# Kernel tuning notes

Hardware: AMD Instinct MI355X
Metric: run time of the kernel (lower is better)

Reference implementation:

```python
import jax, jax.numpy as jnp
import numpy as np

B, N, M, C, T, HF, WF = 4, 512, 32, 512, 8, 14, 14
K = 80          # num_classes
P = 7           # ROI pool output size
HID = 1024
IMG = 224


def setup_inputs() -> dict:
    key = jax.random.key(0)
    k0, k1, k2, k3, k4, k5 = jax.random.split(key, 6)
    feature = jax.random.normal(k0, (B, C, T, HF, WF), dtype=jnp.float32)
    # GT boxes: realistic xyxy boxes inside a 224x224 image
    ka, kb = jax.random.split(k1)
    cxy = jax.random.uniform(ka, (B, M, 2), minval=40.0, maxval=180.0)
    wh = jax.random.uniform(kb, (B, M, 2), minval=40.0, maxval=100.0)
    gt_bboxes = jnp.concatenate([cxy - wh / 2, cxy + wh / 2], axis=-1).astype(jnp.float32)
    # Proposals: jittered copies of GT boxes so many pass the IoU>=0.85 fg test
    idx = jnp.arange(N) % M
    base = gt_bboxes[:, idx]                                   # [B,N,4]
    noise = jax.random.normal(k2, (B, N, 4), dtype=jnp.float32) * 1.5
    proposal_bboxes = jnp.clip(base + noise, 0.0, float(IMG))
    gt_classes = (jax.random.uniform(k3, (B, M, K)) < 0.1).astype(jnp.float32)
    W1 = jax.random.normal(k4, (C * P * P, HID), dtype=jnp.float32) * 0.01
    b1 = jnp.zeros((HID,), jnp.float32)
    W2 = jax.random.normal(k5, (HID, K), dtype=jnp.float32) * 0.01
    b2 = jnp.zeros((K,), jnp.float32)
    return {"feature": feature, "proposal_bboxes": proposal_bboxes,
            "gt_bboxes": gt_bboxes, "gt_classes": gt_classes,
            "W1": W1, "b1": b1, "W2": W2, "b2": b2,
            "image_h": IMG, "image_w": IMG}


def _iou(a, b):
    # a [B,N,4], b [B,M,4] xyxy -> [B,N,M]
    lt = jnp.maximum(a[:, :, None, :2], b[:, None, :, :2])
    rb = jnp.minimum(a[:, :, None, 2:], b[:, None, :, 2:])
    wh = jnp.clip(rb - lt, 0.0)
    inter = wh[..., 0] * wh[..., 1]
    area_a = (a[..., 2] - a[..., 0]) * (a[..., 3] - a[..., 1])
    area_b = (b[..., 2] - b[..., 0]) * (b[..., 3] - b[..., 1])
    return inter / (area_a[:, :, None] + area_b[:, None, :] - inter + 1e-8)


def _roi_pool(feat_bhwc, boxes, bidx, sy, sx):
    # feat_bhwc [B,H,W,C]; boxes [R,4] image coords; bilinear 7x7 ROI pooling
    H, W = feat_bhwc.shape[1], feat_bhwc.shape[2]
    x1, y1, x2, y2 = boxes[:, 0] * sx, boxes[:, 1] * sy, boxes[:, 2] * sx, boxes[:, 3] * sy
    g = (jnp.arange(P, dtype=jnp.float32) + 0.5) / P
    ys = y1[:, None] + g[None, :] * (y2 - y1)[:, None]        # [R,P]
    xs = x1[:, None] + g[None, :] * (x2 - x1)[:, None]        # [R,P]
    y = jnp.broadcast_to(ys[:, :, None], (boxes.shape[0], P, P)) - 0.5
    x = jnp.broadcast_to(xs[:, None, :], (boxes.shape[0], P, P)) - 0.5
    y0f = jnp.floor(y); x0f = jnp.floor(x)
    wy = jnp.clip(y - y0f, 0.0, 1.0)[..., None]
    wx = jnp.clip(x - x0f, 0.0, 1.0)[..., None]
    y0 = jnp.clip(y0f, 0, H - 1).astype(jnp.int32)
    y1i = jnp.clip(y0f + 1, 0, H - 1).astype(jnp.int32)
    x0 = jnp.clip(x0f, 0, W - 1).astype(jnp.int32)
    x1i = jnp.clip(x0f + 1, 0, W - 1).astype(jnp.int32)
    bi = bidx[:, None, None]
    gather = lambda yy, xx: feat_bhwc[bi, yy, xx]             # [R,P,P,C]
    out = (gather(y0, x0) * (1 - wy) * (1 - wx) + gather(y0, x1i) * (1 - wy) * wx +
           gather(y1i, x0) * wy * (1 - wx) + gather(y1i, x1i) * wy * wx)
    return out


def reference(feature, proposal_bboxes, gt_bboxes, gt_classes, W1, b1, W2, b2, image_h, image_w):
    # temporal average pool (AvgPool3d over T) -> [B,C,HF,WF]
    feat = feature.mean(axis=2)
    feat_bhwc = jnp.transpose(feat, (0, 2, 3, 1))             # [B,HF,WF,C]
    # IoU-based fg assignment
    ious = _iou(proposal_bboxes, gt_bboxes)                   # [B,N,M]
    max_iou = ious.max(axis=2)                                # [B,N]
    assign = ious.argmax(axis=2)                              # [B,N]
    any_fg = jnp.any(max_iou >= 0.85)
    thresh = jnp.where(any_fg, 0.85, 0.5)                     # fallback branch
    fg = (max_iou >= thresh).astype(feature.dtype)            # [B,N]
    # ROI pool all proposals (bg masked out in the loss)
    boxes = proposal_bboxes.reshape(B * N, 4)
    bidx = jnp.repeat(jnp.arange(B, dtype=jnp.int32), N)
    sy = feat.shape[2] / float(image_h)
    sx = feat.shape[3] / float(image_w)
    pool = _roi_pool(feat_bhwc, boxes, bidx, sy, sx)          # [R,P,P,C]
    pool = jnp.transpose(pool, (0, 3, 1, 2)).reshape(B * N, C * P * P)
    hidden = jax.nn.relu(pool @ W1 + b1)                      # [R,HID]
    logits = hidden @ W2 + b2                                 # [R,K]
    # multilabel soft-margin labels per proposal
    labels = gt_classes[jnp.repeat(jnp.arange(B), N), assign.reshape(-1)]  # [R,K]
    per = -(labels * jax.nn.log_sigmoid(logits) +
            (1.0 - labels) * jax.nn.log_sigmoid(-logits)).mean(axis=-1)    # [R]
    per = per.reshape(B, N)
    cnt = fg.sum(axis=1)
    losses = jnp.where(cnt > 0, (per * fg).sum(axis=1) / jnp.maximum(cnt, 1.0), 0.0)
    return losses
```

## Files before the change

kernel.cpp:

```cpp
#include <hip/hip_runtime.h>
#include <cstdint>
#include <cstddef>

#define KTOT 25088
#define NBOX 2048
#define HID  1024

typedef __bf16 bf16x8 __attribute__((ext_vector_type(8)));
typedef float  f32x4  __attribute__((ext_vector_type(4)));

__device__ __forceinline__ unsigned short f2bf(float f) {
  union { float f; unsigned u; } v; v.f = f;
  unsigned r = v.u + 0x7FFFu + ((v.u >> 16) & 1u);
  return (unsigned short)(r >> 16);
}

__device__ __forceinline__ float scalar_f(const void* p) {
  int iv = *(const int*)p;
  if (iv > 0 && iv < (1 << 20)) return (float)iv;
  return *(const float*)p;
}

__global__ __launch_bounds__(256) void k_meant(const float* __restrict__ feature,
                                               float* __restrict__ fbhwc) {
  int id = blockIdx.x * 256 + threadIdx.x;
  if (id >= 4 * 512 * 196) return;
  int pix = id % 196;
  int c   = (id / 196) & 511;
  int b   = id / (196 * 512);
  const float* p = feature + ((size_t)(b * 512 + c) * 8) * 196 + pix;
  float s = 0.f;
#pragma unroll
  for (int t = 0; t < 8; ++t) s += p[t * 196];
  fbhwc[((size_t)(b * 196 + pix)) * 512 + c] = s * 0.125f;
}

__global__ __launch_bounds__(256) void k_iou(const float* __restrict__ prop,
                                             const float* __restrict__ gtb,
                                             float* __restrict__ max_iou,
                                             int* __restrict__ assign,
                                             int* __restrict__ flag) {
  __shared__ float g[128];
  int gid = blockIdx.x * 256 + threadIdx.x;
  int b = gid >> 9;
  if (threadIdx.x < 128) g[threadIdx.x] = gtb[b * 128 + threadIdx.x];
  __syncthreads();
  float x1 = prop[gid * 4 + 0], y1 = prop[gid * 4 + 1];
  float x2 = prop[gid * 4 + 2], y2 = prop[gid * 4 + 3];
  float aa = (x2 - x1) * (y2 - y1);
  float best = -1e30f; int arg = 0;
  for (int m = 0; m < 32; ++m) {
    float gx1 = g[m*4], gy1 = g[m*4+1], gx2 = g[m*4+2], gy2 = g[m*4+3];
    float iw = fmaxf(fminf(x2, gx2) - fmaxf(x1, gx1), 0.f);
    float ih = fmaxf(fminf(y2, gy2) - fmaxf(y1, gy1), 0.f);
    float inter = iw * ih;
    float ab = (gx2 - gx1) * (gy2 - gy1);
    float iou = inter / (aa + ab - inter + 1e-8f);
    if (iou > best) { best = iou; arg = m; }
  }
  max_iou[gid] = best; assign[gid] = arg;
  if (best >= 0.85f) atomicOr(flag, 1);
}

__global__ __launch_bounds__(256) void k_w1t(const float* __restrict__ W1,
                                             unsigned short* __restrict__ W1T) {
  __shared__ unsigned short tile[64][68];
  int kp0 = blockIdx.x * 64;
  int h0  = blockIdx.y * 64;
  int t = threadIdx.x;
  int seg = t & 15, ro = t >> 4;
#pragma unroll
  for (int r = 0; r < 4; ++r) {
    int i = ro + r * 16;
    int kp = kp0 + i;
    int srow = (kp & 511) * 49 + (kp >> 9);
    float4 v = *(const float4*)(W1 + (size_t)srow * 1024 + h0 + seg * 4);
    tile[i][seg*4+0] = f2bf(v.x);
    tile[i][seg*4+1] = f2bf(v.y);
    tile[i][seg*4+2] = f2bf(v.z);
    tile[i][seg*4+3] = f2bf(v.w);
  }
  __syncthreads();
#pragma unroll
  for (int r = 0; r < 4; ++r) {
    int hi = ro + r * 16;
    unsigned a = tile[seg*4+0][hi];
    unsigned b = tile[seg*4+1][hi];
    unsigned c = tile[seg*4+2][hi];
    unsigned d = tile[seg*4+3][hi];
    *(uint2*)(W1T + (size_t)(h0+hi)*KTOT + kp0 + seg*4) =
        make_uint2(a | (b << 16), c | (d << 16));
  }
}

__global__ __launch_bounds__(256) void k_roipool(const float* __restrict__ fbhwc,
                                                 const float* __restrict__ prop,
                                                 const void* ihp, const void* iwp,
                                                 unsigned short* __restrict__ Apool) {
  int n = blockIdx.x;
  int tid = threadIdx.x;
  float sy = 14.f / scalar_f(ihp);
  float sx = 14.f / scalar_f(iwp);
  float bx1 = prop[n*4+0]*sx, by1 = prop[n*4+1]*sy;
  float bx2 = prop[n*4+2]*sx, by2 = prop[n*4+3]*sy;
  const float* fb = fbhwc + (size_t)(n >> 9) * 196 * 512;
  unsigned short* arow = Apool + (size_t)n * KTOT;
  int c4 = (tid & 127) << 2;
  int bh = tid >> 7;
  for (int b2i = 0; b2i < 49; b2i += 2) {
    int bin = b2i + bh;
    if (bin >= 49) continue;
    int py = bin / 7, px = bin - py * 7;
    float y = by1 + ((py + 0.5f) * (1.f/7.f)) * (by2 - by1) - 0.5f;
    float x = bx1 + ((px + 0.5f) * (1.f/7.f)) * (bx2 - bx1) - 0.5f;
    float y0f = floorf(y), x0f = floorf(x);
    float wy = y - y0f, wx = x - x0f;
    int y0  = min(max((int)y0f, 0), 13);
    int y1i = min(max((int)y0f + 1, 0), 13);
    int x0  = min(max((int)x0f, 0), 13);
    int x1i = min(max((int)x0f + 1, 0), 13);
    float w00 = (1.f - wy) * (1.f - wx), w01 = (1.f - wy) * wx;
    float w10 = wy * (1.f - wx),         w11 = wy * wx;
    const float4 f00 = *(const float4*)(fb + (y0 * 14 + x0 ) * 512 + c4);
    const float4 f01 = *(const float4*)(fb + (y0 * 14 + x1i) * 512 + c4);
    const float4 f10 = *(const float4*)(fb + (y1i * 14 + x0 ) * 512 + c4);
    const float4 f11 = *(const float4*)(fb + (y1i * 14 + x1i) * 512 + c4);
    float vx = f00.x*w00 + f01.x*w01 + f10.x*w10 + f11.x*w11;
    float vy = f00.y*w00 + f01.y*w01 + f10.y*w10 + f11.y*w11;
    float vz = f00.z*w00 + f01.z*w01 + f10.z*w10 + f11.z*w11;
    float vw = f00.w*w00 + f01.w*w01 + f10.w*w10 + f11.w*w11;
    unsigned lo = (unsigned)f2bf(vx) | ((unsigned)f2bf(vy) << 16);
    unsigned hi = (unsigned)f2bf(vz) | ((unsigned)f2bf(vw) << 16);
    *(uint2*)(arow + bin * 512 + c4) = make_uint2(lo, hi);
  }
}

__device__ __forceinline__ void gload16(const unsigned short* g, unsigned short* l) {
  __builtin_amdgcn_global_load_lds(
      (const __attribute__((address_space(1))) unsigned int*)g,
      (__attribute__((address_space(3))) unsigned int*)l, 16, 0, 0);
}

__global__ __launch_bounds__(512, 2) void k_gemm1(
    const unsigned short* __restrict__ A,
    const unsigned short* __restrict__ B,
    unsigned short* __restrict__ hp)
{
  extern __shared__ unsigned short lds[];
  const int tid  = threadIdx.x;
  const int w    = tid >> 6;
  const int lane = tid & 63;
  const int l15  = lane & 15;
  const int wr = w >> 2, wc = w & 3;
  const int bid = (int)blockIdx.x;
  const int wg  = (bid & 7) * 32 + (bid >> 3);
  const int kb  = wg >> 5;
  const int gy  = (wg >> 2) & 7;
  const int gx  = wg & 3;

  f32x4 acc[8][4];
  const f32x4 zero = {0.f, 0.f, 0.f, 0.f};
#pragma unroll
  for (int m = 0; m < 8; ++m)
#pragma unroll
    for (int n = 0; n < 4; ++n) acc[m][n] = zero;

  const int xsw  = (tid & 7) ^ ((tid >> 3) & 7);
  const int rloc = ((tid >> 3) << 1) + (xsw >> 2);
  const int qsrc = xsw & 3;
  const size_t kbase = (size_t)kb * 3136;
  const unsigned short* gAp = A + (size_t)(gy * 256 + rloc) * KTOT + kbase + qsrc * 8;
  const unsigned short* gBp = B + (size_t)(gx * 256 + rloc) * KTOT + kbase + qsrc * 8;
  const int dstc = tid * 8;

  const int pfr   = ((lane >> 4) | ((l15 & 1) << 2)) ^ (l15 >> 1);
  const int aoffc = wr * 4096 + (l15 >> 1) * 64 + pfr * 8;
  const int boffc = wc * 2048 + (l15 >> 1) * 64 + pfr * 8;

  bf16x8 Afr[8], Bfr[4];

#define STG(SLOT, KN) { \
    gload16(gAp + (KN),                      lds + (SLOT)*16384 + dstc); \
    gload16(gAp + (KN) + (size_t)128 * KTOT, lds + (SLOT)*16384 + 4096 + dstc); \
    gload16(gBp + (KN),                      lds + (SLOT)*16384 + 8192 + dstc); \
    gload16(gBp + (KN) + (size_t)128 * KTOT, lds + (SLOT)*16384 + 12288 + dstc); }
#define LDA(i, SLOT) Afr[i] = *reinterpret_cast<const bf16x8*>( \
    lds + (SLOT)*16384 + aoffc + (i)*512);
#define LDB(n, SLOT) Bfr[n] = *reinterpret_cast<const bf16x8*>( \
    lds + (SLOT)*16384 + 8192 + boffc + (n)*512);
#define VM4 asm volatile("s_waitcnt vmcnt(4)" ::: "memory");
#define VM0 asm volatile("s_waitcnt vmcnt(0)" ::: "memory");
#define VMN

#define STEP(CS, DOSTG, KN, VMASM, DOREFILL)                                   \
  {                                                                            \
    if (DOSTG) STG((((CS)+2)&3), KN)                                           \
    VMASM                                                                      \
    __builtin_amdgcn_s_barrier();                                              \
    __builtin_amdgcn_s_setprio(1);                                             \
    _Pragma("unroll") for (int i = 0; i < 8; ++i) {                            \
      _Pragma("unroll") for (int n = 0; n < 4; ++n)                            \
        acc[i][n] = __builtin_amdgcn_mfma_f32_16x16x32_bf16(                   \
            Afr[i], Bfr[n], acc[i][n], 0, 0, 0);                               \
      if (DOREFILL) LDA(i, (((CS)+1)&3))                                       \
    }                                                                          \
    if (DOREFILL) { _Pragma("unroll") for (int n = 0; n < 4; ++n)              \
                      LDB(n, (((CS)+1)&3)) }                                   \
    __builtin_amdgcn_s_setprio(0);                                             \
  }

  STG(0, 0)
  STG(1, 32)
  VM4
  __builtin_amdgcn_s_barrier();
#pragma unroll
  for (int i = 0; i < 8; ++i) LDA(i, 0)
#pragma unroll
  for (int n = 0; n < 4; ++n) LDB(n, 0)

#pragma unroll 1
  for (int s4 = 0; s4 < 96; s4 += 4) {
    STEP(0, true, (size_t)(s4 + 2) * 32, VM4, true)
    STEP(1, true, (size_t)(s4 + 3) * 32, VM4, true)
    STEP(2, true, (size_t)(s4 + 4) * 32, VM4, true)
    STEP(3, true, (size_t)(s4 + 5) * 32, VM4, true)
  }
  STEP(0, false, 0, VM0, true)
  STEP(1, false, 0, VMN, false)

#undef STEP
#undef VMN
#undef VM0
#undef VM4
#undef LDB
#undef LDA
#undef STG

  unsigned short* o = hp + (size_t)kb * (2048u * 1024u);
  const int r0 = gy * 256 + wr * 128 + ((lane >> 4) << 2);
  const int c0 = gx * 256 + wc * 64 + l15;
#pragma unroll
  for (int m = 0; m < 8; ++m)
#pragma unroll
    for (int n = 0; n < 4; ++n)
#pragma unroll
      for (int j = 0; j < 4; ++j)
        o[(size_t)(r0 + m * 16 + j) * 1024 + c0 + n * 16] = f2bf(acc[m][n][j]);
}

template<int OUTBF>
__global__ __launch_bounds__(256, 4) void k_gemm(
    const unsigned short* __restrict__ A,
    const unsigned short* __restrict__ B,
    void* __restrict__ outp,
    int Kst, int kIters, int nTileBits, int mTileBits, int ldc)
{
  __shared__ unsigned short As[2][4096];
  __shared__ unsigned short Bs[2][4096];
  const int tid  = threadIdx.x;
  const int w    = tid >> 6;
  const int lane = tid & 63;
  const int nwg = (int)gridDim.x, cpx = nwg >> 3;
  const int bid = (int)blockIdx.x;
  const int wg  = (bid & 7) * cpx + (bid >> 3);
  const int kb  = wg >> (mTileBits + nTileBits);
  const int rem = wg & ((1 << (mTileBits + nTileBits)) - 1);
  const int gy  = rem >> nTileBits;
  const int gx  = rem & ((1 << nTileBits) - 1);
  const int wr = w >> 1, wc = w & 1;

  f32x4 acc[4][4];
  const f32x4 zero = {0.f, 0.f, 0.f, 0.f};
#pragma unroll
  for (int m = 0; m < 4; ++m)
#pragma unroll
    for (int n = 0; n < 4; ++n) acc[m][n] = zero;

  const int r0   = 32 * w + (lane >> 2);
  const int qsrc = (lane & 3) ^ ((lane >> 3) & 3);
  const size_t kbase = (size_t)kb * kIters * 32;
  const unsigned short* gA = A + (size_t)(gy * 128 + r0) * Kst + kbase + qsrc * 8;
  const unsigned short* gB = B + (size_t)(gx * 128 + r0) * Kst + kbase + qsrc * 8;
  const int ldst = r0 * 32 + (lane & 3) * 8;

  const int swq = ((lane >> 4) ^ ((lane >> 1) & 3)) * 8;
  const int ar = (wr * 64 + (lane & 15)) * 32 + swq;
  const int br = (wc * 64 + (lane & 15)) * 32 + swq;

#define STAGE(bufi, it) do {                                         \
    const unsigned short* pa = gA + (size_t)(it) * 32;               \
    const unsigned short* pb = gB + (size_t)(it) * 32;               \
    gload16(pa,                      &As[bufi][ldst]);               \
    gload16(pa + (size_t)16 * Kst,   &As[bufi][ldst + 512]);         \
    gload16(pb,                      &Bs[bufi][ldst]);               \
    gload16(pb + (size_t)16 * Kst,   &Bs[bufi][ldst + 512]);         \
  } while (0)

  STAGE(0, 0);
  int cur = 0;
  for (int kk = 0; kk < kIters; ++kk) {
    __syncthreads();
    if (kk + 1 < kIters) STAGE(cur ^ 1, kk + 1);
    bf16x8 af[4], bfr[4];
#pragma unroll
    for (int m = 0; m < 4; ++m)
      af[m] = *reinterpret_cast<const bf16x8*>(&As[cur][ar + m * 512]);
#pragma unroll
    for (int n = 0; n < 4; ++n)
      bfr[n] = *reinterpret_cast<const bf16x8*>(&Bs[cur][br + n * 512]);
#pragma unroll
    for (int m = 0; m < 4; ++m)
#pragma unroll
      for (int n = 0; n < 4; ++n)
        acc[m][n] = __builtin_amdgcn_mfma_f32_16x16x32_bf16(af[m], bfr[n], acc[m][n], 0, 0, 0);
    cur ^= 1;
  }
#undef STAGE

  const size_t M = (size_t)(1 << mTileBits) * 128;
  const size_t splitStride = M * (size_t)ldc;
  const int r0o = gy * 128 + wr * 64 + ((lane >> 4) << 2);
  const int c0o = gx * 128 + wc * 64 + (lane & 15);
  if (OUTBF) {
    unsigned short* o = (unsigned short*)outp + (size_t)kb * splitStride;
#pragma unroll
    for (int m = 0; m < 4; ++m)
#pragma unroll
      for (int n = 0; n < 4; ++n)
#pragma unroll
        for (int j = 0; j < 4; ++j)
          o[(size_t)(r0o + m * 16 + j) * ldc + c0o + n * 16] = f2bf(acc[m][n][j]);
  } else {
    float* o = (float*)outp + (size_t)kb * splitStride;
#pragma unroll
    for (int m = 0; m < 4; ++m)
#pragma unroll
      for (int n = 0; n < 4; ++n)
#pragma unroll
        for (int j = 0; j < 4; ++j)
          o[(size_t)(r0o + m * 16 + j) * ldc + c0o + n * 16] = acc[m][n][j];
  }
}

__global__ __launch_bounds__(256) void k_combine(const unsigned short* __restrict__ hp,
                                                 const float* __restrict__ b1,
                                                 unsigned short* __restrict__ hidden) {
  int gid = blockIdx.x * 256 + threadIdx.x;
  int id8 = gid * 8;
  int h = id8 & 1023;
  float a[8];
#pragma unroll
  for (int j = 0; j < 8; ++j) a[j] = b1[h + j];
#pragma unroll
  for (int s = 0; s < 8; ++s) {
    uint4 u = *(const uint4*)(hp + (size_t)s * 2097152 + id8);
    unsigned uu[4] = {u.x, u.y, u.z, u.w};
#pragma unroll
    for (int q = 0; q < 4; ++q) {
      union { unsigned u; float f; } lo, hi;
      lo.u = uu[q] << 16; hi.u = uu[q] & 0xFFFF0000u;
      a[2*q]   += lo.f;
      a[2*q+1] += hi.f;
    }
  }
  unsigned out[4];
#pragma unroll
  for (int q = 0; q < 4; ++q) {
    unsigned l  = f2bf(fmaxf(a[2*q],   0.f));
    unsigned hh = f2bf(fmaxf(a[2*q+1], 0.f));
    out[q] = l | (hh << 16);
  }
  *(uint4*)(hidden + id8) = make_uint4(out[0], out[1], out[2], out[3]);
}

__global__ __launch_bounds__(256) void k_w2t(const float* __restrict__ W2,
                                             unsigned short* __restrict__ W2T) {
  int id = blockIdx.x * 256 + threadIdx.x;
  int cls = id >> 10, k = id & 1023;
  float v = (cls < 80) ? W2[(size_t)k * 80 + cls] : 0.f;
  W2T[id] = f2bf(v);
}

__global__ __launch_bounds__(256) void k_bce(const float* __restrict__ hp2,
                                             const float* __restrict__ b2,
                                             const float* __restrict__ gtc,
                                             const int* __restrict__ assign,
                                             float* __restrict__ per) {
  __shared__ float red[256];
  int t = threadIdx.x;
  int box = t >> 4, li = t & 15;
  int n = blockIdx.x * 16 + box;
  int lab = ((n >> 9) * 32 + assign[n]) * 80;
  float s = 0.f;
#pragma unroll
  for (int j = 0; j < 5; ++j) {
    int c = li + 16 * j;
    size_t o = (size_t)n * 128 + c;
    float x = hp2[o] + hp2[o + 262144] + hp2[o + 524288] + hp2[o + 786432] + b2[c];
    float y = gtc[lab + c];
    float ce = log1pf(expf(-fabsf(x)));
    s += y * (fmaxf(-x, 0.f) + ce) + (1.f - y) * (fmaxf(x, 0.f) + ce);
  }
  red[t] = s;
  __syncthreads();
  if (li == 0) {
    float tot = 0.f;
#pragma unroll
    for (int i = 0; i < 16; ++i) tot += red[box * 16 + i];
    per[n] = tot * (1.f / 80.f);
  }
}

__global__ __launch_bounds__(512) void k_reduce(const float* __restrict__ per,
                                                const float* __restrict__ max_iou,
                                                const int* __restrict__ flag,
                                                float* __restrict__ out) {
  __shared__ float sv[8], sf[8];
  int b = blockIdx.x, tid = threadIdx.x;
  float thr = (*flag) ? 0.85f : 0.5f;
  int n = b * 512 + tid;
  float f = (max_iou[n] >= thr) ? 1.f : 0.f;
  float v = per[n] * f;
#pragma unroll
  for (int o = 32; o > 0; o >>= 1) {
    v += __shfl_down(v, o);
    f += __shfl_down(f, o);
  }
  int wv = tid >> 6;
  if ((tid & 63) == 0) { sv[wv] = v; sf[wv] = f; }
  __syncthreads();
  if (tid == 0) {
    float S = 0.f, F = 0.f;
#pragma unroll
    for (int i = 0; i < 8; ++i) { S += sv[i]; F += sf[i]; }
    out[b] = (F > 0.f) ? S / fmaxf(F, 1.f) : 0.f;
  }
}

extern "C" void kernel_launch(void* const* d_in, const int* in_sizes, int n_in,
                              void* d_out, int out_size, void* d_ws, size_t ws_size,
                              hipStream_t stream) {
  const float* feature = (const float*)d_in[0];
  const float* prop    = (const float*)d_in[1];
  const float* gtb     = (const float*)d_in[2];
  const float* gtc     = (const float*)d_in[3];
  const float* W1      = (const float*)d_in[4];
  const float* b1      = (const float*)d_in[5];
  const float* W2      = (const float*)d_in[6];
  const float* b2      = (const float*)d_in[7];
  const void*  ihp     = d_in[8];
  const void*  iwp     = d_in[9];

  char* ws = (char*)d_ws;
  float*          fbhwc  = (float*)(ws);
  unsigned short* W1T    = (unsigned short*)(ws + 1605632);
  unsigned short* Apool  = (unsigned short*)(ws + 52985856);
  unsigned short* hp     = (unsigned short*)(ws + 155746304);
  float*          max_iou= (float*)(ws + 189300736);
  int*            assign = (int*)(ws + 189308928);
  float*          per    = (float*)(ws + 189317120);
  int*            flag   = (int*)(ws + 189325312);
  unsigned short* hidden = W1T;
  unsigned short* W2T    = Apool;
  float*          hp2    = (float*)((char*)Apool + 262144);

  hipFuncSetAttribute((const void*)k_gemm1,
                      hipFuncAttributeMaxDynamicSharedMemorySize, 131072);

  hipMemsetAsync(flag, 0, sizeof(int), stream);
  k_meant  <<<1568, 256, 0, stream>>>(feature, fbhwc);
  k_iou    <<<8, 256, 0, stream>>>(prop, gtb, max_iou, assign, flag);
  k_w1t    <<<dim3(392, 16), 256, 0, stream>>>(W1, W1T);
  k_roipool<<<2048, 256, 0, stream>>>(fbhwc, prop, ihp, iwp, Apool);
  k_gemm1  <<<256, 512, 131072, stream>>>(Apool, W1T, hp);
  k_combine<<<1024, 256, 0, stream>>>(hp, b1, hidden);
  k_w2t    <<<512, 256, 0, stream>>>(W2, W2T);
  k_gemm<0><<<64, 256, 0, stream>>>(hidden, W2T, hp2, 1024, 8, 0, 4, 128);
  k_bce    <<<128, 256, 0, stream>>>(hp2, b2, gtc, assign, per);
  k_reduce <<<4, 512, 0, stream>>>(per, max_iou, flag, (float*)d_out);
}
```

Before: 202.8 us.

## Merge W1 transpose and ROI pool, double-buffer B fragments, split GEMM2 over more K

Merges the W1 transpose/convert kernel and the ROI-pool kernel into a single launch that picks its role from the block index, saving one launch and letting the two run side by side. In the main GEMM, B fragments are double-buffered so the next step's B loads are issued right after the barrier and overlap the MFMAs, at the cost of extra registers. The second GEMM now splits K eight ways over 128 blocks, and the BCE kernel sums eight partial outputs instead of four.

```diff
diff --git a/kernel.cpp b/kernel.cpp
--- a/kernel.cpp
+++ b/kernel.cpp
@@ -62,76 +62,75 @@
   if (best >= 0.85f) atomicOr(flag, 1);
 }
 
-__global__ __launch_bounds__(256) void k_w1t(const float* __restrict__ W1,
-                                             unsigned short* __restrict__ W1T) {
+__global__ __launch_bounds__(256) void k_prep(
+    const float* __restrict__ W1, unsigned short* __restrict__ W1T,
+    const float* __restrict__ fbhwc, const float* __restrict__ prop,
+    const void* ihp, const void* iwp, unsigned short* __restrict__ Apool) {
   __shared__ unsigned short tile[64][68];
-  int kp0 = blockIdx.x * 64;
-  int h0  = blockIdx.y * 64;
+  int blk = blockIdx.x;
   int t = threadIdx.x;
-  int seg = t & 15, ro = t >> 4;
-#pragma unroll
-  for (int r = 0; r < 4; ++r) {
-    int i = ro + r * 16;
-    int kp = kp0 + i;
-    int srow = (kp & 511) * 49 + (kp >> 9);
-    float4 v = *(const float4*)(W1 + (size_t)srow * 1024 + h0 + seg * 4);
-    tile[i][seg*4+0] = f2bf(v.x);
-    tile[i][seg*4+1] = f2bf(v.y);
-    tile[i][seg*4+2] = f2bf(v.z);
-    tile[i][seg*4+3] = f2bf(v.w);
-  }
-  __syncthreads();
-#pragma unroll
-  for (int r = 0; r < 4; ++r) {
-    int hi = ro + r * 16;
-    unsigned a = tile[seg*4+0][hi];
-    unsigned b = tile[seg*4+1][hi];
-    unsigned c = tile[seg*4+2][hi];
-    unsigned d = tile[seg*4+3][hi];
-    *(uint2*)(W1T + (size_t)(h0+hi)*KTOT + kp0 + seg*4) =
-        make_uint2(a | (b << 16), c | (d << 16));
-  }
-}
-
-__global__ __launch_bounds__(256) void k_roipool(const float* __restrict__ fbhwc,
-                                                 const float* __restrict__ prop,
-                                                 const void* ihp, const void* iwp,
-                                                 unsigned short* __restrict__ Apool) {
-  int n = blockIdx.x;
-  int tid = threadIdx.x;
-  float sy = 14.f / scalar_f(ihp);
-  float sx = 14.f / scalar_f(iwp);
-  float bx1 = prop[n*4+0]*sx, by1 = prop[n*4+1]*sy;
-  float bx2 = prop[n*4+2]*sx, by2 = prop[n*4+3]*sy;
-  const float* fb = fbhwc + (size_t)(n >> 9) * 196 * 512;
-  unsigned short* arow = Apool + (size_t)n * KTOT;
-  int c4 = (tid & 127) << 2;
-  int bh = tid >> 7;
-  for (int b2i = 0; b2i < 49; b2i += 2) {
-    int bin = b2i + bh;
-    if (bin >= 49) continue;
-    int py = bin / 7, px = bin - py * 7;
-    float y = by1 + ((py + 0.5f) * (1.f/7.f)) * (by2 - by1) - 0.5f;
-    float x = bx1 + ((px + 0.5f) * (1.f/7.f)) * (bx2 - bx1) - 0.5f;
-    float y0f = floorf(y), x0f = floorf(x);
-    float wy = y - y0f, wx = x - x0f;
-    int y0  = min(max((int)y0f, 0), 13);
-    int y1i = min(max((int)y0f + 1, 0), 13);
-    int x0  = min(max((int)x0f, 0), 13);
-    int x1i = min(max((int)x0f + 1, 0), 13);
-    float w00 = (1.f - wy) * (1.f - wx), w01 = (1.f - wy) * wx;
-    float w10 = wy * (1.f - wx),         w11 = wy * wx;
-    const float4 f00 = *(const float4*)(fb + (y0 * 14 + x0 ) * 512 + c4);
-    const float4 f01 = *(const float4*)(fb + (y0 * 14 + x1i) * 512 + c4);
-    const float4 f10 = *(const float4*)(fb + (y1i * 14 + x0 ) * 512 + c4);
-    const float4 f11 = *(const float4*)(fb + (y1i * 14 + x1i) * 512 + c4);
-    float vx = f00.x*w00 + f01.x*w01 + f10.x*w10 + f11.x*w11;
-    float vy = f00.y*w00 + f01.y*w01 + f10.y*w10 + f11.y*w11;
-    float vz = f00.z*w00 + f01.z*w01 + f10.z*w10 + f11.z*w11;
-    float vw = f00.w*w00 + f01.w*w01 + f10.w*w10 + f11.w*w11;
-    unsigned lo = (unsigned)f2bf(vx) | ((unsigned)f2bf(vy) << 16);
-    unsigned hi = (unsigned)f2bf(vz) | ((unsigned)f2bf(vw) << 16);
-    *(uint2*)(arow + bin * 512 + c4) = make_uint2(lo, hi);
+  if (blk < 6272) {
+    int kp0 = (blk % 392) * 64;
+    int h0  = (blk / 392) * 64;
+    int seg = t & 15, ro = t >> 4;
+#pragma unroll
+    for (int r = 0; r < 4; ++r) {
+      int i = ro + r * 16;
+      int kp = kp0 + i;
+      int srow = (kp & 511) * 49 + (kp >> 9);
+      float4 v = *(const float4*)(W1 + (size_t)srow * 1024 + h0 + seg * 4);
+      tile[i][seg*4+0] = f2bf(v.x);
+      tile[i][seg*4+1] = f2bf(v.y);
+      tile[i][seg*4+2] = f2bf(v.z);
+      tile[i][seg*4+3] = f2bf(v.w);
+    }
+    __syncthreads();
+#pragma unroll
+    for (int r = 0; r < 4; ++r) {
+      int hi = ro + r * 16;
+      unsigned a = tile[seg*4+0][hi];
+      unsigned b = tile[seg*4+1][hi];
+      unsigned c = tile[seg*4+2][hi];
+      unsigned d = tile[seg*4+3][hi];
+      *(uint2*)(W1T + (size_t)(h0+hi)*KTOT + kp0 + seg*4) =
+          make_uint2(a | (b << 16), c | (d << 16));
+    }
+  } else {
+    int n = blk - 6272;
+    float sy = 14.f / scalar_f(ihp);
+    float sx = 14.f / scalar_f(iwp);
+    float bx1 = prop[n*4+0]*sx, by1 = prop[n*4+1]*sy;
+    float bx2 = prop[n*4+2]*sx, by2 = prop[n*4+3]*sy;
+    const float* fb = fbhwc + (size_t)(n >> 9) * 196 * 512;
+    unsigned short* arow = Apool + (size_t)n * KTOT;
+    int c4 = (t & 127) << 2;
+    int bh = t >> 7;
+    for (int b2i = 0; b2i < 49; b2i += 2) {
+      int bin = b2i + bh;
+      if (bin >= 49) continue;
+      int py = bin / 7, px = bin - py * 7;
+      float y = by1 + ((py + 0.5f) * (1.f/7.f)) * (by2 - by1) - 0.5f;
+      float x = bx1 + ((px + 0.5f) * (1.f/7.f)) * (bx2 - bx1) - 0.5f;
+      float y0f = floorf(y), x0f = floorf(x);
+      float wy = y - y0f, wx = x - x0f;
+      int y0  = min(max((int)y0f, 0), 13);
+      int y1i = min(max((int)y0f + 1, 0), 13);
+      int x0  = min(max((int)x0f, 0), 13);
+      int x1i = min(max((int)x0f + 1, 0), 13);
+      float w00 = (1.f - wy) * (1.f - wx), w01 = (1.f - wy) * wx;
+      float w10 = wy * (1.f - wx),         w11 = wy * wx;
+      const float4 f00 = *(const float4*)(fb + (y0 * 14 + x0 ) * 512 + c4);
+      const float4 f01 = *(const float4*)(fb + (y0 * 14 + x1i) * 512 + c4);
+      const float4 f10 = *(const float4*)(fb + (y1i * 14 + x0 ) * 512 + c4);
+      const float4 f11 = *(const float4*)(fb + (y1i * 14 + x1i) * 512 + c4);
+      float vx = f00.x*w00 + f01.x*w01 + f10.x*w10 + f11.x*w11;
+      float vy = f00.y*w00 + f01.y*w01 + f10.y*w10 + f11.y*w11;
+      float vz = f00.z*w00 + f01.z*w01 + f10.z*w10 + f11.z*w11;
+      float vw = f00.w*w00 + f01.w*w01 + f10.w*w10 + f11.w*w11;
+      unsigned lo = (unsigned)f2bf(vx) | ((unsigned)f2bf(vy) << 16);
+      unsigned hi = (unsigned)f2bf(vz) | ((unsigned)f2bf(vw) << 16);
+      *(uint2*)(arow + bin * 512 + c4) = make_uint2(lo, hi);
+    }
   }
 }
 
@@ -177,7 +176,7 @@
   const int aoffc = wr * 4096 + (l15 >> 1) * 64 + pfr * 8;
   const int boffc = wc * 2048 + (l15 >> 1) * 64 + pfr * 8;
 
-  bf16x8 Afr[8], Bfr[4];
+  bf16x8 Afr[8], B0[4], B1[4];
 
 #define STG(SLOT, KN) { \
     gload16(gAp + (KN),                      lds + (SLOT)*16384 + dstc); \
@@ -186,26 +185,26 @@
     gload16(gBp + (KN) + (size_t)128 * KTOT, lds + (SLOT)*16384 + 12288 + dstc); }
 #define LDA(i, SLOT) Afr[i] = *reinterpret_cast<const bf16x8*>( \
     lds + (SLOT)*16384 + aoffc + (i)*512);
-#define LDB(n, SLOT) Bfr[n] = *reinterpret_cast<const bf16x8*>( \
+#define LDBx(arr, n, SLOT) arr[n] = *reinterpret_cast<const bf16x8*>( \
     lds + (SLOT)*16384 + 8192 + boffc + (n)*512);
 #define VM4 asm volatile("s_waitcnt vmcnt(4)" ::: "memory");
 #define VM0 asm volatile("s_waitcnt vmcnt(0)" ::: "memory");
 #define VMN
 
-#define STEP(CS, DOSTG, KN, VMASM, DOREFILL)                                   \
+#define STEP(BC, BN, CS, DOSTG, KN, VMASM, DOREFILL)                           \
   {                                                                            \
     if (DOSTG) STG((((CS)+2)&3), KN)                                           \
     VMASM                                                                      \
     __builtin_amdgcn_s_barrier();                                              \
+    if (DOREFILL) { _Pragma("unroll") for (int n = 0; n < 4; ++n)              \
+                      LDBx(BN, n, (((CS)+1)&3)) }                              \
     __builtin_amdgcn_s_setprio(1);                                             \
     _Pragma("unroll") for (int i = 0; i < 8; ++i) {                            \
       _Pragma("unroll") for (int n = 0; n < 4; ++n)                            \
         acc[i][n] = __builtin_amdgcn_mfma_f32_16x16x32_bf16(                   \
-            Afr[i], Bfr[n], acc[i][n], 0, 0, 0);                               \
+            Afr[i], BC[n], acc[i][n], 0, 0, 0);                                \
       if (DOREFILL) LDA(i, (((CS)+1)&3))                                       \
     }                                                                          \
-    if (DOREFILL) { _Pragma("unroll") for (int n = 0; n < 4; ++n)              \
-                      LDB(n, (((CS)+1)&3)) }                                   \
     __builtin_amdgcn_s_setprio(0);                                             \
   }
 
@@ -216,23 +215,23 @@
 #pragma unroll
   for (int i = 0; i < 8; ++i) LDA(i, 0)
 #pragma unroll
-  for (int n = 0; n < 4; ++n) LDB(n, 0)
+  for (int n = 0; n < 4; ++n) LDBx(B0, n, 0)
 
 #pragma unroll 1
   for (int s4 = 0; s4 < 96; s4 += 4) {
-    STEP(0, true, (size_t)(s4 + 2) * 32, VM4, true)
-    STEP(1, true, (size_t)(s4 + 3) * 32, VM4, true)
-    STEP(2, true, (size_t)(s4 + 4) * 32, VM4, true)
-    STEP(3, true, (size_t)(s4 + 5) * 32, VM4, true)
-  }
-  STEP(0, false, 0, VM0, true)
-  STEP(1, false, 0, VMN, false)
+    STEP(B0, B1, 0, true, (size_t)(s4 + 2) * 32, VM4, true)
+    STEP(B1, B0, 1, true, (size_t)(s4 + 3) * 32, VM4, true)
+    STEP(B0, B1, 2, true, (size_t)(s4 + 4) * 32, VM4, true)
+    STEP(B1, B0, 3, true, (size_t)(s4 + 5) * 32, VM4, true)
+  }
+  STEP(B0, B1, 0, false, 0, VM0, true)
+  STEP(B1, B0, 1, false, 0, VMN, false)
 
 #undef STEP
 #undef VMN
 #undef VM0
 #undef VM4
-#undef LDB
+#undef LDBx
 #undef LDA
 #undef STG
 
@@ -396,7 +395,9 @@
   for (int j = 0; j < 5; ++j) {
     int c = li + 16 * j;
     size_t o = (size_t)n * 128 + c;
-    float x = hp2[o] + hp2[o + 262144] + hp2[o + 524288] + hp2[o + 786432] + b2[c];
+    float x = b2[c];
+#pragma unroll
+    for (int sp = 0; sp < 8; ++sp) x += hp2[o + (size_t)sp * 262144];
     float y = gtc[lab + c];
     float ce = log1pf(expf(-fabsf(x)));
     s += y * (fmaxf(-x, 0.f) + ce) + (1.f - y) * (fmaxf(x, 0.f) + ce);
@@ -470,12 +471,11 @@
   hipMemsetAsync(flag, 0, sizeof(int), stream);
   k_meant  <<<1568, 256, 0, stream>>>(feature, fbhwc);
   k_iou    <<<8, 256, 0, stream>>>(prop, gtb, max_iou, assign, flag);
-  k_w1t    <<<dim3(392, 16), 256, 0, stream>>>(W1, W1T);
-  k_roipool<<<2048, 256, 0, stream>>>(fbhwc, prop, ihp, iwp, Apool);
+  k_prep   <<<8320, 256, 0, stream>>>(W1, W1T, fbhwc, prop, ihp, iwp, Apool);
   k_gemm1  <<<256, 512, 131072, stream>>>(Apool, W1T, hp);
   k_combine<<<1024, 256, 0, stream>>>(hp, b1, hidden);
   k_w2t    <<<512, 256, 0, stream>>>(W2, W2T);
-  k_gemm<0><<<64, 256, 0, stream>>>(hidden, W2T, hp2, 1024, 8, 0, 4, 128);
+  k_gemm<0><<<128, 256, 0, stream>>>(hidden, W2T, hp2, 1024, 4, 0, 4, 128);
   k_bce    <<<128, 256, 0, stream>>>(hp2, b2, gtc, assign, per);
   k_reduce <<<4, 512, 0, stream>>>(per, max_iou, flag, (float*)d_out);
 }
```

Measured after the change: 194.8 us. 1.04x faster.
